# Kernel optimization log

Hardware: AMD Instinct MI355X
Metric: run time of the kernel (lower is better)

## Reference

```python
import jax, jax.numpy as jnp
import numpy as np
from jax import lax

HIDDEN = 256      # hidden_dim
LATENT = 128      # latent_dim
VOCAB = 32000     # vocab_size
MAX_LEN = 64      # max_len (stack capacity guard, as in original)
MAX_STEPS = 128   # fixed step budget for the decode stack machine
N_NODES = 511     # complete binary tree, depth 9


def _linear_params(key, fan_in, fan_out):
    k1, k2 = jax.random.split(key)
    s = 1.0 / np.sqrt(fan_in)
    W = jax.random.uniform(k1, (fan_out, fan_in), minval=-s, maxval=s, dtype=jnp.float32)
    b = jax.random.uniform(k2, (fan_out,), minval=-s, maxval=s, dtype=jnp.float32)
    return W, b


def setup_inputs() -> dict:
    key = jax.random.key(0)
    ks = jax.random.split(key, 10)
    embed = jax.random.normal(ks[0], (VOCAB, HIDDEN), dtype=jnp.float32)
    Wpar, bpar = _linear_params(ks[1], 3 * HIDDEN, HIDDEN)
    Wmu, bmu = _linear_params(ks[2], HIDDEN, LATENT)
    Wlv, blv = _linear_params(ks[3], HIDDEN, LATENT)
    W1, b1 = _linear_params(ks[4], LATENT, HIDDEN)
    W2, b2 = _linear_params(ks[5], HIDDEN, HIDDEN + 1)
    Wl, bl = _linear_params(ks[6], HIDDEN, VOCAB)
    Wp, bp = _linear_params(ks[7], HIDDEN, 2 * LATENT + VOCAB)
    values = jax.random.randint(ks[8], (N_NODES,), 0, VOCAB)
    idx = np.arange(N_NODES)
    left = np.where(2 * idx + 1 < N_NODES, 2 * idx + 1, -1).astype(np.int32)
    right = np.where(2 * idx + 2 < N_NODES, 2 * idx + 2, -1).astype(np.int32)
    eps = jax.random.normal(ks[9], (LATENT,), dtype=jnp.float32)
    return dict(embed=embed, Wpar=Wpar, bpar=bpar, Wmu=Wmu, bmu=bmu,
                Wlv=Wlv, blv=blv, W1=W1, b1=b1, W2=W2, b2=b2,
                Wl=Wl, bl=bl, Wp=Wp, bp=bp, eps=eps,
                values=jnp.asarray(values), left=jnp.asarray(left), right=jnp.asarray(right))


def reference(embed, Wpar, bpar, Wmu, bmu, Wlv, blv, W1, b1, W2, b2,
              Wl, bl, Wp, bp, eps, values, left, right):
    # ---------- encode: bottom-up over tree stored as index arrays ----------
    emb = embed[values]  # [N, H], one gather for all node embeddings

    def enc_step(h, i):
        v = emb[i]
        li = jnp.maximum(left[i], 0)
        ri = jnp.maximum(right[i], 0)
        cat = jnp.concatenate([v, h[li], h[ri]])          # [3H]
        hp = cat @ Wpar.T + bpar                           # parent combine
        hi = jnp.where(left[i] < 0, v, hp)                 # leaf -> embedding
        return h.at[i].set(hi), None

    h0 = jnp.zeros((values.shape[0], HIDDEN), dtype=embed.dtype)
    # children have larger index than parents -> process in descending order
    h, _ = lax.scan(enc_step, h0, jnp.arange(values.shape[0] - 1, -1, -1))
    root = h[0]
    mu = root @ Wmu.T + bmu
    logvar = root @ Wlv.T + blv
    z = mu + eps * jnp.exp(0.5 * logvar)                   # reparameterize

    # ---------- decode: stack machine with fixed step budget ----------
    V, L = VOCAB, LATENT
    stack0 = jnp.zeros((MAX_LEN, L), dtype=z.dtype).at[0].set(z)
    out0 = jnp.zeros((MAX_STEPS, V), dtype=z.dtype)

    def dec_step(state, _):
        stack, sp, out, op = state
        active = sp > 0
        idx = jnp.maximum(sp - 1, 0)
        node = stack[idx]                                  # pop
        hmid = jax.nn.leaky_relu(node @ W1.T + b1, 0.2)
        co = hmid @ W2.T + b2                              # [H+1]; co[0] = gate
        is_parent = (co[0] > 0) & (sp - 1 <= MAX_LEN - 2) & active

        def parent_fn(_):
            dec = co[1:] @ Wp.T + bp                       # [V + 2L]
            value = dec[:V]
            ll = dec[V:V + L]
            rl = dec[V + L:]
            # original appends llatent then rlatent -> rlatent on top
            st = stack.at[idx].set(ll).at[idx + 1].set(rl)
            return value, st, sp + 1

        def leaf_fn(_):
            return co[1:] @ Wl.T + bl, stack, sp - 1

        value, st, nsp = lax.cond(is_parent, parent_fn, leaf_fn, None)
        m = active.astype(z.dtype)
        out = out.at[op].add(m * value)                    # rows written once
        stack = jnp.where(active, st, stack)
        sp = jnp.where(active, nsp, sp)
        op = op + active.astype(op.dtype)
        return (stack, sp, out, op), None

    init = (stack0, jnp.int32(1), out0, jnp.int32(0))
    (_, _, out, _), _ = lax.scan(dec_step, init, None, length=MAX_STEPS)
    return out, mu, logvar
```

## Files before the change

### kernel.cpp

```cpp
#include <hip/hip_runtime.h>

#define HID 256
#define LAT 128
#define VOC 32000
#define NSTEP 128

__global__ __launch_bounds__(512)
void prep_kernel(const float* __restrict__ Wp, const float* __restrict__ W2,
                 const float* __restrict__ b2, const float* __restrict__ bp,
                 const float* __restrict__ Wpar,
                 const float* __restrict__ Wmu, const float* __restrict__ Wlv,
                 float* __restrict__ Wcomb, float* __restrict__ bcomb,
                 float* __restrict__ Wq_par, float* __restrict__ Wq_mu,
                 float* __restrict__ Wq_lv, float* __restrict__ Wq_w2) {
    const int b = blockIdx.x;
    const int t = threadIdx.x;
    if (b < 256) {
        const int o = b;
        const int k = t & 255, jh = t >> 8;
        __shared__ float wpt_s[256];
        __shared__ float part_s[2][256];
        __shared__ float red_s[4];
        if (t < 256) wpt_s[t] = Wp[(size_t)(VOC + o) * HID + t];
        __syncthreads();
        float acc = 0.f;
#pragma unroll 8
        for (int j = 0; j < 128; j++)
            acc += wpt_s[jh * 128 + j] * W2[(size_t)(1 + jh * 128 + j) * HID + k];
        part_s[jh][k] = acc;
        if (t < 256) {
            float p = wpt_s[k] * b2[1 + k];
            p += __shfl_xor(p, 1);  p += __shfl_xor(p, 2);  p += __shfl_xor(p, 4);
            p += __shfl_xor(p, 8);  p += __shfl_xor(p, 16); p += __shfl_xor(p, 32);
            if ((k & 63) == 0) red_s[k >> 6] = p;
        }
        __syncthreads();
        if (t < 256) Wcomb[(size_t)o * HID + k] = part_s[0][k] + part_s[1][k];
        if (t == 0) bcomb[o] = bp[VOC + o] + red_s[0] + red_s[1] + red_s[2] + red_s[3];
    } else if (b < 352) {
        const int k4 = (b - 256) * 2 + (t >> 8);
        const int r = t & 255;
        ((float4*)Wq_par)[k4 * 256 + r] = *(const float4*)(Wpar + (size_t)r * 768 + 4 * k4);
    } else if (b < 384) {
        const int k4 = (b - 352) * 2 + (t >> 8);
        const int r = t & 127, sel = (t >> 7) & 1;
        const float* src = (sel ? Wlv : Wmu) + (size_t)r * HID + 4 * k4;
        ((float4*)(sel ? Wq_lv : Wq_mu))[k4 * 128 + r] = *(const float4*)src;
    } else {
        const int k4 = (b - 384) * 2 + (t >> 8);
        const int r = t & 255;
        ((float4*)Wq_w2)[k4 * 256 + r] = *(const float4*)(W2 + (size_t)(1 + r) * HID + 4 * k4);
    }
}

__global__ __launch_bounds__(1024)
void enc2(const float* __restrict__ embed, const int* __restrict__ values,
          const float* __restrict__ Wq, const float* __restrict__ bpar,
          float* __restrict__ h, int base) {
    const int i = base + blockIdx.x;
    const int t = threadIdx.x;
    const int o = t & 255;
    const int g = t >> 8;
    const int cid = g & 1, kh = g >> 1;
    __shared__ __align__(16) float cat[2][768];
    __shared__ float part[4][256];
    __shared__ __align__(16) float pcat[768];

    const int c0n = 2 * i + 1;
    for (int q = t; q < 1536; q += 1024) {
        const int cc = (q >= 768);
        const int e = q - cc * 768;
        const int node = c0n + cc;
        const int seg = e >> 8, idx = e & 255;
        float v;
        if (seg == 0) v = embed[(size_t)values[node] * HID + idx];
        else {
            const int ch = 2 * node + seg;
            v = (ch >= 255) ? embed[(size_t)values[ch] * HID + idx]
                            : h[(size_t)ch * HID + idx];
        }
        cat[cc][e] = v;
    }
    __syncthreads();
    {
        const float4* wq = (const float4*)Wq + o;
        const float4* c4 = (const float4*)cat[cid] + kh * 96;
        float acc = 0.f;
#pragma unroll 16
        for (int k4 = 0; k4 < 96; k4++) {
            const float4 w = wq[(size_t)(kh * 96 + k4) * 256];
            const float4 cc = c4[k4];
            acc += w.x * cc.x + w.y * cc.y + w.z * cc.z + w.w * cc.w;
        }
        part[g][o] = acc;
    }
    __syncthreads();
    if (t < 512) {
        const int c = t >> 8;
        pcat[256 + (c << 8) + o] = part[c][o] + part[c + 2][o] + bpar[o];
    } else if (t < 768) {
        const int idx = t & 255;
        pcat[idx] = embed[(size_t)values[i] * HID + idx];
    }
    __syncthreads();
    {
        const float4* wq = (const float4*)Wq + o;
        const float4* c4 = (const float4*)pcat + g * 48;
        float acc = 0.f;
#pragma unroll 16
        for (int k4 = 0; k4 < 48; k4++) {
            const float4 w = wq[(size_t)(g * 48 + k4) * 256];
            const float4 cc = c4[k4];
            acc += w.x * cc.x + w.y * cc.y + w.z * cc.z + w.w * cc.w;
        }
        part[g][o] = acc;
    }
    __syncthreads();
    if (t < 256)
        h[(size_t)i * HID + t] = part[0][t] + part[1][t] + part[2][t] + part[3][t] + bpar[t];
}

__global__ __launch_bounds__(1024)
void enc_final(const float* __restrict__ embed, const int* __restrict__ values,
               const float* __restrict__ Wq, const float* __restrict__ bpar,
               const float* __restrict__ h,
               const float* __restrict__ Wq_mu, const float* __restrict__ bmu,
               const float* __restrict__ Wq_lv, const float* __restrict__ blv,
               const float* __restrict__ eps,
               float* __restrict__ out, float* __restrict__ z) {
    const int t = threadIdx.x;
    const int o = t & 255;
    const int g = t >> 8;
    const int cid = g & 1, kh = g >> 1;
    __shared__ __align__(16) float cat[2][768];
    __shared__ float part[4][256];
    __shared__ __align__(16) float pcat[768];
    __shared__ __align__(16) float r0[256];
    __shared__ float mu_s[128], lv_s[128];

    for (int q = t; q < 1536; q += 1024) {
        const int cc = (q >= 768);
        const int e = q - cc * 768;
        const int node = 1 + cc;
        const int seg = e >> 8, idx = e & 255;
        cat[cc][e] = (seg == 0) ? embed[(size_t)values[node] * HID + idx]
                                : h[(size_t)(2 * node + seg) * HID + idx];
    }
    __syncthreads();
    {
        const float4* wq = (const float4*)Wq + o;
        const float4* c4 = (const float4*)cat[cid] + kh * 96;
        float acc = 0.f;
#pragma unroll 16
        for (int k4 = 0; k4 < 96; k4++) {
            const float4 w = wq[(size_t)(kh * 96 + k4) * 256];
            const float4 cc = c4[k4];
            acc += w.x * cc.x + w.y * cc.y + w.z * cc.z + w.w * cc.w;
        }
        part[g][o] = acc;
    }
    __syncthreads();
    if (t < 512) {
        const int c = t >> 8;
        pcat[256 + (c << 8) + o] = part[c][o] + part[c + 2][o] + bpar[o];
    } else if (t < 768) {
        const int idx = t & 255;
        pcat[idx] = embed[(size_t)values[0] * HID + idx];
    }
    __syncthreads();
    {
        const float4* wq = (const float4*)Wq + o;
        const float4* c4 = (const float4*)pcat + g * 48;
        float acc = 0.f;
#pragma unroll 16
        for (int k4 = 0; k4 < 48; k4++) {
            const float4 w = wq[(size_t)(g * 48 + k4) * 256];
            const float4 cc = c4[k4];
            acc += w.x * cc.x + w.y * cc.y + w.z * cc.z + w.w * cc.w;
        }
        part[g][o] = acc;
    }
    __syncthreads();
    if (t < 256)
        r0[t] = part[0][t] + part[1][t] + part[2][t] + part[3][t] + bpar[t];
    __syncthreads();
    {
        const int r = o & 127;
        const float4* wqh = (const float4*)(o < 128 ? Wq_mu : Wq_lv) + r;
        const float4* r4 = (const float4*)r0 + g * 16;
        float acc = 0.f;
#pragma unroll 16
        for (int k4 = 0; k4 < 16; k4++) {
            const float4 w = wqh[(size_t)(g * 16 + k4) * 128];
            const float4 cc = r4[k4];
            acc += w.x * cc.x + w.y * cc.y + w.z * cc.z + w.w * cc.w;
        }
        part[g][o] = acc;
    }
    __syncthreads();
    if (t < 256) {
        const int r = t & 127;
        float v = part[0][t] + part[1][t] + part[2][t] + part[3][t];
        if (t < 128) { v += bmu[r]; out[(size_t)NSTEP * VOC + r] = v;       mu_s[r] = v; }
        else         { v += blv[r]; out[(size_t)NSTEP * VOC + 128 + r] = v; lv_s[r] = v; }
    }
    __syncthreads();
    if (t < 128) z[t] = mu_s[t] + eps[t] * expf(0.5f * lv_s[t]);
}

__global__ __launch_bounds__(512, 2)
void recur_kernel(const float* W1, const float* b1,
                  const float* W2, const float* b2,
                  const float* Wcomb, const float* bcomb,
                  const float* z,
                  float* Hrec, int* rowflag) {
    const int t = threadIdx.x;
    const int o = t >> 1;
    const int hk = t & 1;
    __shared__ __align__(16) float stack_s[64 * 128];
    __shared__ __align__(16) float hmid_s[256];

    float4 w1r[16];
#pragma unroll
    for (int j = 0; j < 16; j++)
        w1r[j] = *(const float4*)(W1 + (size_t)o * 128 + hk * 64 + 4 * j);
    float4 wcr[32];
#pragma unroll
    for (int j = 0; j < 32; j++)
        wcr[j] = *(const float4*)(Wcomb + (size_t)o * 256 + hk * 128 + 4 * j);

    const float b1o = b1[o];
    const float bco = bcomb[o];
    const float b20 = b2[0];
    const int l64 = t & 63;
    const float4 w2q = *(const float4*)(W2 + 4 * l64);

    if (t < 128) stack_s[t] = z[t];
    int sp = 1, op = 0;
    unsigned long long pm0 = 0ULL, pm1 = 0ULL;
    __syncthreads();

    for (int step = 0; step < NSTEP; step++) {
        if (sp <= 0) break;
        const int idx = sp - 1;

        const float* np = stack_s + idx * 128 + hk * 64;
        float a = 0.f;
#pragma unroll
        for (int j = 0; j < 16; j++) {
            const float4 v = *(const float4*)(np + 4 * j);
            a += w1r[j].x * v.x + w1r[j].y * v.y + w1r[j].z * v.z + w1r[j].w * v.w;
        }
        a += __shfl_xor(a, 1);
        if (hk == 0) {
            float pre = a + b1o;
            pre = pre > 0.f ? pre : 0.2f * pre;
            hmid_s[o] = pre;
            Hrec[(size_t)op * HID + o] = pre;
        }
        __syncthreads();

        const float4 hq = *(const float4*)(hmid_s + 4 * l64);
        float c = w2q.x * hq.x + w2q.y * hq.y + w2q.z * hq.z + w2q.w * hq.w;
        c += __shfl_xor(c, 1);  c += __shfl_xor(c, 2);  c += __shfl_xor(c, 4);
        c += __shfl_xor(c, 8);  c += __shfl_xor(c, 16); c += __shfl_xor(c, 32);
        const bool par = ((c + b20) > 0.f) && (sp <= 63);

        if (par) {
            const float* hp = hmid_s + hk * 128;
            float s = 0.f;
#pragma unroll
            for (int j = 0; j < 32; j++) {
                const float4 v = *(const float4*)(hp + 4 * j);
                s += wcr[j].x * v.x + wcr[j].y * v.y + wcr[j].z * v.z + wcr[j].w * v.w;
            }
            s += __shfl_xor(s, 1);
            if (hk == 0)
                stack_s[(idx + (o >> 7)) * 128 + (o & 127)] = s + bco;
            if (op < 64) pm0 |= (1ULL << op); else pm1 |= (1ULL << (op - 64));
            sp += 1;
        } else {
            sp -= 1;
        }
        op++;
        __syncthreads();
    }

    if (t < 128) {
        int f = -1;
        if (t < op) f = (t < 64) ? (int)((pm0 >> t) & 1) : (int)((pm1 >> (t - 64)) & 1);
        rowflag[t] = f;
    }
}

__global__ __launch_bounds__(256)
void co1_kernel(const float* __restrict__ Hrec, const float* __restrict__ Wq_w2,
                const float* __restrict__ b2, float* __restrict__ Co1) {
    const int r = blockIdx.x;
    const int c = threadIdx.x;
    __shared__ __align__(16) float hs[256];
    hs[c] = Hrec[(size_t)r * HID + c];
    __syncthreads();
    float acc = b2[1 + c];
    const float4* wq = (const float4*)Wq_w2 + c;
    const float4* h4 = (const float4*)hs;
#pragma unroll 8
    for (int k4 = 0; k4 < 64; k4++) {
        const float4 a = wq[k4 * 256];
        const float4 hv = h4[k4];
        acc += a.x * hv.x + a.y * hv.y + a.z * hv.z + a.w * hv.w;
    }
    Co1[(size_t)r * HID + c] = acc;
}

__global__ __launch_bounds__(256, 1)
void value_kernel(const float* __restrict__ Co1, const int* __restrict__ rowflag,
                  const float* __restrict__ Wl, const float* __restrict__ bl,
                  const float* __restrict__ Wp, const float* __restrict__ bp,
                  float* __restrict__ out) {
    const int m = blockIdx.y;
    const int t = threadIdx.x;
    const int v = blockIdx.x * 256 + t;
    __shared__ int list_s[128];
    __shared__ int zlist_s[128];
    __shared__ int nn_s, nz_s;
    if (t == 0) {
        int n = 0, znum = 0;
        for (int r = 0; r < 128; r++) {
            const int f = rowflag[r];
            if (f == m) list_s[n++] = r;
            else if (m == 0 && f == -1) zlist_s[znum++] = r;
        }
        nn_s = n; nz_s = znum;
    }
    __syncthreads();
    const int n = nn_s;
    const float* Wx = m ? Wp : Wl;
    const float* bx = m ? bp : bl;
    const float bv = bx[v];
    const float4* w4 = (const float4*)(Wx + (size_t)v * HID);

    for (int rc = 0; rc < n; rc += 32) {
        const int nr = min(32, n - rc);
        float acc[32];
#pragma unroll
        for (int rr = 0; rr < 32; rr++) acc[rr] = 0.f;
        for (int kc = 0; kc < 4; kc++) {
            float4 w[16];
#pragma unroll
            for (int i = 0; i < 16; i++) w[i] = w4[kc * 16 + i];
            for (int rr = 0; rr < nr; rr++) {
                const int row = __builtin_amdgcn_readfirstlane(list_s[rc + rr]);
                const float* cp = Co1 + (size_t)row * HID + kc * 64;
                float s = 0.f;
#pragma unroll
                for (int i = 0; i < 16; i++) {
                    const float4 c4 = *(const float4*)(cp + 4 * i);
                    s += w[i].x * c4.x + w[i].y * c4.y + w[i].z * c4.z + w[i].w * c4.w;
                }
                acc[rr] += s;
            }
        }
        for (int rr = 0; rr < nr; rr++) {
            const int row = __builtin_amdgcn_readfirstlane(list_s[rc + rr]);
            out[(size_t)row * VOC + v] = acc[rr] + bv;
        }
    }
    if (m == 0) {
        const int nz = nz_s;
        for (int i = 0; i < nz; i++) {
            const int row = __builtin_amdgcn_readfirstlane(zlist_s[i]);
            out[(size_t)row * VOC + v] = 0.f;
        }
    }
}

extern "C" void kernel_launch(void* const* d_in, const int* in_sizes, int n_in,
                              void* d_out, int out_size, void* d_ws, size_t ws_size,
                              hipStream_t stream) {
    const float* embed = (const float*)d_in[0];
    const float* Wpar  = (const float*)d_in[1];
    const float* bpar  = (const float*)d_in[2];
    const float* Wmu   = (const float*)d_in[3];
    const float* bmu   = (const float*)d_in[4];
    const float* Wlv   = (const float*)d_in[5];
    const float* blv   = (const float*)d_in[6];
    const float* W1    = (const float*)d_in[7];
    const float* b1    = (const float*)d_in[8];
    const float* W2    = (const float*)d_in[9];
    const float* b2    = (const float*)d_in[10];
    const float* Wl    = (const float*)d_in[11];
    const float* bl    = (const float*)d_in[12];
    const float* Wp    = (const float*)d_in[13];
    const float* bp    = (const float*)d_in[14];
    const float* eps   = (const float*)d_in[15];
    const int*  values = (const int*)d_in[16];

    float* ws = (float*)d_ws;
    float* h       = ws;
    float* z       = ws + 65280;
    float* Wcomb   = ws + 65408;
    float* bcomb   = ws + 130944;
    float* Hrec    = ws + 131200;
    float* Co1     = ws + 163968;
    int*   rowflag = (int*)(ws + 196736);
    float* Wq_par  = ws + 196864;
    float* Wq_mu   = ws + 393472;
    float* Wq_lv   = ws + 426240;
    float* Wq_w2   = ws + 459008;
    float* out = (float*)d_out;

    prep_kernel<<<416, 512, 0, stream>>>(Wp, W2, b2, bp, Wpar, Wmu, Wlv,
                                         Wcomb, bcomb, Wq_par, Wq_mu, Wq_lv, Wq_w2);

    enc2<<<64, 1024, 0, stream>>>(embed, values, Wq_par, bpar, h, 63);
    enc2<<<16, 1024, 0, stream>>>(embed, values, Wq_par, bpar, h, 15);
    enc2<<< 4, 1024, 0, stream>>>(embed, values, Wq_par, bpar, h,  3);
    enc_final<<<1, 1024, 0, stream>>>(embed, values, Wq_par, bpar, h,
                                      Wq_mu, bmu, Wq_lv, blv, eps, out, z);

    recur_kernel<<<1, 512, 0, stream>>>(W1, b1, W2, b2, Wcomb, bcomb, z, Hrec, rowflag);

    co1_kernel<<<128, 256, 0, stream>>>(Hrec, Wq_w2, b2, Co1);
    value_kernel<<<dim3(125, 2), 256, 0, stream>>>(Co1, rowflag, Wl, bl, Wp, bp, out);
}
```

Measured before the change: 281.2 us.

## Split dot-product accumulators, precompute row lists, and double value-kernel grid

Every dot-product loop (encoder, recurrence, co1, value) now uses several independent fmaf accumulators to shorten the serial add chains. Building the row lists by a single thread moves out of each value_kernel block into an extra block of co1_kernel, which writes them to workspace. value_kernel now covers 128 vocab columns per block and splits rows across two thread halves, doubling the grid to fill more compute units. The trade-offs are a different float summation order and more redundant weight loads per column, since both thread halves load the same weights.

```diff
diff --git a/kernel.cpp b/kernel.cpp
--- a/kernel.cpp
+++ b/kernel.cpp
@@ -85,14 +85,24 @@
     {
         const float4* wq = (const float4*)Wq + o;
         const float4* c4 = (const float4*)cat[cid] + kh * 96;
-        float acc = 0.f;
-#pragma unroll 16
-        for (int k4 = 0; k4 < 96; k4++) {
-            const float4 w = wq[(size_t)(kh * 96 + k4) * 256];
-            const float4 cc = c4[k4];
-            acc += w.x * cc.x + w.y * cc.y + w.z * cc.z + w.w * cc.w;
-        }
-        part[g][o] = acc;
+        float s0 = 0.f, s1 = 0.f, s2 = 0.f, s3 = 0.f;
+#pragma unroll 8
+        for (int k4 = 0; k4 < 96; k4 += 4) {
+            const float4 wa = wq[(size_t)(kh * 96 + k4) * 256];
+            const float4 wb = wq[(size_t)(kh * 96 + k4 + 1) * 256];
+            const float4 wc = wq[(size_t)(kh * 96 + k4 + 2) * 256];
+            const float4 wd = wq[(size_t)(kh * 96 + k4 + 3) * 256];
+            const float4 ca = c4[k4], cb = c4[k4 + 1], cx = c4[k4 + 2], cd = c4[k4 + 3];
+            s0 = fmaf(wa.x, ca.x, s0); s0 = fmaf(wa.y, ca.y, s0);
+            s0 = fmaf(wa.z, ca.z, s0); s0 = fmaf(wa.w, ca.w, s0);
+            s1 = fmaf(wb.x, cb.x, s1); s1 = fmaf(wb.y, cb.y, s1);
+            s1 = fmaf(wb.z, cb.z, s1); s1 = fmaf(wb.w, cb.w, s1);
+            s2 = fmaf(wc.x, cx.x, s2); s2 = fmaf(wc.y, cx.y, s2);
+            s2 = fmaf(wc.z, cx.z, s2); s2 = fmaf(wc.w, cx.w, s2);
+            s3 = fmaf(wd.x, cd.x, s3); s3 = fmaf(wd.y, cd.y, s3);
+            s3 = fmaf(wd.z, cd.z, s3); s3 = fmaf(wd.w, cd.w, s3);
+        }
+        part[g][o] = (s0 + s1) + (s2 + s3);
     }
     __syncthreads();
     if (t < 512) {
@@ -106,14 +116,24 @@
     {
         const float4* wq = (const float4*)Wq + o;
         const float4* c4 = (const float4*)pcat + g * 48;
-        float acc = 0.f;
-#pragma unroll 16
-        for (int k4 = 0; k4 < 48; k4++) {
-            const float4 w = wq[(size_t)(g * 48 + k4) * 256];
-            const float4 cc = c4[k4];
-            acc += w.x * cc.x + w.y * cc.y + w.z * cc.z + w.w * cc.w;
-        }
-        part[g][o] = acc;
+        float s0 = 0.f, s1 = 0.f, s2 = 0.f, s3 = 0.f;
+#pragma unroll
+        for (int k4 = 0; k4 < 48; k4 += 4) {
+            const float4 wa = wq[(size_t)(g * 48 + k4) * 256];
+            const float4 wb = wq[(size_t)(g * 48 + k4 + 1) * 256];
+            const float4 wc = wq[(size_t)(g * 48 + k4 + 2) * 256];
+            const float4 wd = wq[(size_t)(g * 48 + k4 + 3) * 256];
+            const float4 ca = c4[k4], cb = c4[k4 + 1], cx = c4[k4 + 2], cd = c4[k4 + 3];
+            s0 = fmaf(wa.x, ca.x, s0); s0 = fmaf(wa.y, ca.y, s0);
+            s0 = fmaf(wa.z, ca.z, s0); s0 = fmaf(wa.w, ca.w, s0);
+            s1 = fmaf(wb.x, cb.x, s1); s1 = fmaf(wb.y, cb.y, s1);
+            s1 = fmaf(wb.z, cb.z, s1); s1 = fmaf(wb.w, cb.w, s1);
+            s2 = fmaf(wc.x, cx.x, s2); s2 = fmaf(wc.y, cx.y, s2);
+            s2 = fmaf(wc.z, cx.z, s2); s2 = fmaf(wc.w, cx.w, s2);
+            s3 = fmaf(wd.x, cd.x, s3); s3 = fmaf(wd.y, cd.y, s3);
+            s3 = fmaf(wd.z, cd.z, s3); s3 = fmaf(wd.w, cd.w, s3);
+        }
+        part[g][o] = (s0 + s1) + (s2 + s3);
     }
     __syncthreads();
     if (t < 256)
@@ -150,14 +170,24 @@
     {
         const float4* wq = (const float4*)Wq + o;
         const float4* c4 = (const float4*)cat[cid] + kh * 96;
-        float acc = 0.f;
-#pragma unroll 16
-        for (int k4 = 0; k4 < 96; k4++) {
-            const float4 w = wq[(size_t)(kh * 96 + k4) * 256];
-            const float4 cc = c4[k4];
-            acc += w.x * cc.x + w.y * cc.y + w.z * cc.z + w.w * cc.w;
-        }
-        part[g][o] = acc;
+        float s0 = 0.f, s1 = 0.f, s2 = 0.f, s3 = 0.f;
+#pragma unroll 8
+        for (int k4 = 0; k4 < 96; k4 += 4) {
+            const float4 wa = wq[(size_t)(kh * 96 + k4) * 256];
+            const float4 wb = wq[(size_t)(kh * 96 + k4 + 1) * 256];
+            const float4 wc = wq[(size_t)(kh * 96 + k4 + 2) * 256];
+            const float4 wd = wq[(size_t)(kh * 96 + k4 + 3) * 256];
+            const float4 ca = c4[k4], cb = c4[k4 + 1], cx = c4[k4 + 2], cd = c4[k4 + 3];
+            s0 = fmaf(wa.x, ca.x, s0); s0 = fmaf(wa.y, ca.y, s0);
+            s0 = fmaf(wa.z, ca.z, s0); s0 = fmaf(wa.w, ca.w, s0);
+            s1 = fmaf(wb.x, cb.x, s1); s1 = fmaf(wb.y, cb.y, s1);
+            s1 = fmaf(wb.z, cb.z, s1); s1 = fmaf(wb.w, cb.w, s1);
+            s2 = fmaf(wc.x, cx.x, s2); s2 = fmaf(wc.y, cx.y, s2);
+            s2 = fmaf(wc.z, cx.z, s2); s2 = fmaf(wc.w, cx.w, s2);
+            s3 = fmaf(wd.x, cd.x, s3); s3 = fmaf(wd.y, cd.y, s3);
+            s3 = fmaf(wd.z, cd.z, s3); s3 = fmaf(wd.w, cd.w, s3);
+        }
+        part[g][o] = (s0 + s1) + (s2 + s3);
     }
     __syncthreads();
     if (t < 512) {
@@ -171,14 +201,24 @@
     {
         const float4* wq = (const float4*)Wq + o;
         const float4* c4 = (const float4*)pcat + g * 48;
-        float acc = 0.f;
-#pragma unroll 16
-        for (int k4 = 0; k4 < 48; k4++) {
-            const float4 w = wq[(size_t)(g * 48 + k4) * 256];
-            const float4 cc = c4[k4];
-            acc += w.x * cc.x + w.y * cc.y + w.z * cc.z + w.w * cc.w;
-        }
-        part[g][o] = acc;
+        float s0 = 0.f, s1 = 0.f, s2 = 0.f, s3 = 0.f;
+#pragma unroll
+        for (int k4 = 0; k4 < 48; k4 += 4) {
+            const float4 wa = wq[(size_t)(g * 48 + k4) * 256];
+            const float4 wb = wq[(size_t)(g * 48 + k4 + 1) * 256];
+            const float4 wc = wq[(size_t)(g * 48 + k4 + 2) * 256];
+            const float4 wd = wq[(size_t)(g * 48 + k4 + 3) * 256];
+            const float4 ca = c4[k4], cb = c4[k4 + 1], cx = c4[k4 + 2], cd = c4[k4 + 3];
+            s0 = fmaf(wa.x, ca.x, s0); s0 = fmaf(wa.y, ca.y, s0);
+            s0 = fmaf(wa.z, ca.z, s0); s0 = fmaf(wa.w, ca.w, s0);
+            s1 = fmaf(wb.x, cb.x, s1); s1 = fmaf(wb.y, cb.y, s1);
+            s1 = fmaf(wb.z, cb.z, s1); s1 = fmaf(wb.w, cb.w, s1);
+            s2 = fmaf(wc.x, cx.x, s2); s2 = fmaf(wc.y, cx.y, s2);
+            s2 = fmaf(wc.z, cx.z, s2); s2 = fmaf(wc.w, cx.w, s2);
+            s3 = fmaf(wd.x, cd.x, s3); s3 = fmaf(wd.y, cd.y, s3);
+            s3 = fmaf(wd.z, cd.z, s3); s3 = fmaf(wd.w, cd.w, s3);
+        }
+        part[g][o] = (s0 + s1) + (s2 + s3);
     }
     __syncthreads();
     if (t < 256)
@@ -188,14 +228,18 @@
         const int r = o & 127;
         const float4* wqh = (const float4*)(o < 128 ? Wq_mu : Wq_lv) + r;
         const float4* r4 = (const float4*)r0 + g * 16;
-        float acc = 0.f;
-#pragma unroll 16
-        for (int k4 = 0; k4 < 16; k4++) {
-            const float4 w = wqh[(size_t)(g * 16 + k4) * 128];
-            const float4 cc = r4[k4];
-            acc += w.x * cc.x + w.y * cc.y + w.z * cc.z + w.w * cc.w;
-        }
-        part[g][o] = acc;
+        float s0 = 0.f, s1 = 0.f;
+#pragma unroll
+        for (int k4 = 0; k4 < 16; k4 += 2) {
+            const float4 wa = wqh[(size_t)(g * 16 + k4) * 128];
+            const float4 wb = wqh[(size_t)(g * 16 + k4 + 1) * 128];
+            const float4 ca = r4[k4], cb = r4[k4 + 1];
+            s0 = fmaf(wa.x, ca.x, s0); s0 = fmaf(wa.y, ca.y, s0);
+            s0 = fmaf(wa.z, ca.z, s0); s0 = fmaf(wa.w, ca.w, s0);
+            s1 = fmaf(wb.x, cb.x, s1); s1 = fmaf(wb.y, cb.y, s1);
+            s1 = fmaf(wb.z, cb.z, s1); s1 = fmaf(wb.w, cb.w, s1);
+        }
+        part[g][o] = s0 + s1;
     }
     __syncthreads();
     if (t < 256) {
@@ -245,12 +289,17 @@
         const int idx = sp - 1;
 
         const float* np = stack_s + idx * 128 + hk * 64;
-        float a = 0.f;
-#pragma unroll
-        for (int j = 0; j < 16; j++) {
-            const float4 v = *(const float4*)(np + 4 * j);
-            a += w1r[j].x * v.x + w1r[j].y * v.y + w1r[j].z * v.z + w1r[j].w * v.w;
-        }
+        float a0 = 0.f, a1 = 0.f;
+#pragma unroll
+        for (int j = 0; j < 16; j += 2) {
+            const float4 v0 = *(const float4*)(np + 4 * j);
+            const float4 v1 = *(const float4*)(np + 4 * j + 4);
+            a0 = fmaf(w1r[j].x, v0.x, a0);     a0 = fmaf(w1r[j].y, v0.y, a0);
+            a0 = fmaf(w1r[j].z, v0.z, a0);     a0 = fmaf(w1r[j].w, v0.w, a0);
+            a1 = fmaf(w1r[j + 1].x, v1.x, a1); a1 = fmaf(w1r[j + 1].y, v1.y, a1);
+            a1 = fmaf(w1r[j + 1].z, v1.z, a1); a1 = fmaf(w1r[j + 1].w, v1.w, a1);
+        }
+        float a = a0 + a1;
         a += __shfl_xor(a, 1);
         if (hk == 0) {
             float pre = a + b1o;
@@ -268,12 +317,23 @@
 
         if (par) {
             const float* hp = hmid_s + hk * 128;
-            float s = 0.f;
-#pragma unroll
-            for (int j = 0; j < 32; j++) {
-                const float4 v = *(const float4*)(hp + 4 * j);
-                s += wcr[j].x * v.x + wcr[j].y * v.y + wcr[j].z * v.z + wcr[j].w * v.w;
+            float s0 = 0.f, s1 = 0.f, s2 = 0.f, s3 = 0.f;
+#pragma unroll
+            for (int j = 0; j < 32; j += 4) {
+                const float4 v0 = *(const float4*)(hp + 4 * j);
+                const float4 v1 = *(const float4*)(hp + 4 * j + 4);
+                const float4 v2 = *(const float4*)(hp + 4 * j + 8);
+                const float4 v3 = *(const float4*)(hp + 4 * j + 12);
+                s0 = fmaf(wcr[j].x, v0.x, s0);     s0 = fmaf(wcr[j].y, v0.y, s0);
+                s0 = fmaf(wcr[j].z, v0.z, s0);     s0 = fmaf(wcr[j].w, v0.w, s0);
+                s1 = fmaf(wcr[j + 1].x, v1.x, s1); s1 = fmaf(wcr[j + 1].y, v1.y, s1);
+                s1 = fmaf(wcr[j + 1].z, v1.z, s1); s1 = fmaf(wcr[j + 1].w, v1.w, s1);
+                s2 = fmaf(wcr[j + 2].x, v2.x, s2); s2 = fmaf(wcr[j + 2].y, v2.y, s2);
+                s2 = fmaf(wcr[j + 2].z, v2.z, s2); s2 = fmaf(wcr[j + 2].w, v2.w, s2);
+                s3 = fmaf(wcr[j + 3].x, v3.x, s3); s3 = fmaf(wcr[j + 3].y, v3.y, s3);
+                s3 = fmaf(wcr[j + 3].z, v3.z, s3); s3 = fmaf(wcr[j + 3].w, v3.w, s3);
             }
+            float s = (s0 + s1) + (s2 + s3);
             s += __shfl_xor(s, 1);
             if (hk == 0)
                 stack_s[(idx + (o >> 7)) * 128 + (o & 127)] = s + bco;
@@ -295,46 +355,58 @@
 
 __global__ __launch_bounds__(256)
 void co1_kernel(const float* __restrict__ Hrec, const float* __restrict__ Wq_w2,
-                const float* __restrict__ b2, float* __restrict__ Co1) {
+                const float* __restrict__ b2, const int* __restrict__ rowflag,
+                float* __restrict__ Co1, int* __restrict__ lists) {
     const int r = blockIdx.x;
     const int c = threadIdx.x;
+    if (r == 128) {
+        if (c == 0) {
+            int nl = 0, np_ = 0, nz = 0;
+            for (int q = 0; q < 128; q++) {
+                const int f = rowflag[q];
+                if (f == 0) lists[nl++] = q;
+                else if (f == 1) lists[128 + np_++] = q;
+                else lists[256 + nz++] = q;
+            }
+            lists[384] = nl; lists[385] = np_; lists[386] = nz;
+        }
+        return;
+    }
     __shared__ __align__(16) float hs[256];
     hs[c] = Hrec[(size_t)r * HID + c];
     __syncthreads();
-    float acc = b2[1 + c];
     const float4* wq = (const float4*)Wq_w2 + c;
     const float4* h4 = (const float4*)hs;
+    float s0 = b2[1 + c], s1 = 0.f, s2 = 0.f, s3 = 0.f;
 #pragma unroll 8
-    for (int k4 = 0; k4 < 64; k4++) {
-        const float4 a = wq[k4 * 256];
-        const float4 hv = h4[k4];
-        acc += a.x * hv.x + a.y * hv.y + a.z * hv.z + a.w * hv.w;
-    }
-    Co1[(size_t)r * HID + c] = acc;
-}
-
-__global__ __launch_bounds__(256, 1)
-void value_kernel(const float* __restrict__ Co1, const int* __restrict__ rowflag,
+    for (int k4 = 0; k4 < 64; k4 += 4) {
+        const float4 a0 = wq[(k4) * 256],     h0 = h4[k4];
+        const float4 a1 = wq[(k4 + 1) * 256], h1 = h4[k4 + 1];
+        const float4 a2 = wq[(k4 + 2) * 256], h2 = h4[k4 + 2];
+        const float4 a3 = wq[(k4 + 3) * 256], h3 = h4[k4 + 3];
+        s0 = fmaf(a0.x, h0.x, s0); s0 = fmaf(a0.y, h0.y, s0);
+        s0 = fmaf(a0.z, h0.z, s0); s0 = fmaf(a0.w, h0.w, s0);
+        s1 = fmaf(a1.x, h1.x, s1); s1 = fmaf(a1.y, h1.y, s1);
+        s1 = fmaf(a1.z, h1.z, s1); s1 = fmaf(a1.w, h1.w, s1);
+        s2 = fmaf(a2.x, h2.x, s2); s2 = fmaf(a2.y, h2.y, s2);
+        s2 = fmaf(a2.z, h2.z, s2); s2 = fmaf(a2.w, h2.w, s2);
+        s3 = fmaf(a3.x, h3.x, s3); s3 = fmaf(a3.y, h3.y, s3);
+        s3 = fmaf(a3.z, h3.z, s3); s3 = fmaf(a3.w, h3.w, s3);
+    }
+    Co1[(size_t)r * HID + c] = (s0 + s1) + (s2 + s3);
+}
+
+__global__ __launch_bounds__(256, 2)
+void value_kernel(const float* __restrict__ Co1, const int* __restrict__ lists,
                   const float* __restrict__ Wl, const float* __restrict__ bl,
                   const float* __restrict__ Wp, const float* __restrict__ bp,
                   float* __restrict__ out) {
     const int m = blockIdx.y;
     const int t = threadIdx.x;
-    const int v = blockIdx.x * 256 + t;
-    __shared__ int list_s[128];
-    __shared__ int zlist_s[128];
-    __shared__ int nn_s, nz_s;
-    if (t == 0) {
-        int n = 0, znum = 0;
-        for (int r = 0; r < 128; r++) {
-            const int f = rowflag[r];
-            if (f == m) list_s[n++] = r;
-            else if (m == 0 && f == -1) zlist_s[znum++] = r;
-        }
-        nn_s = n; nz_s = znum;
-    }
-    __syncthreads();
-    const int n = nn_s;
+    const int v = blockIdx.x * 128 + (t & 127);
+    const int rh = t >> 7;
+    const int n = lists[384 + m];
+    const int* list = lists + m * 128;
     const float* Wx = m ? Wp : Wl;
     const float* bx = m ? bp : bl;
     const float bv = bx[v];
@@ -342,36 +414,53 @@
 
     for (int rc = 0; rc < n; rc += 32) {
         const int nr = min(32, n - rc);
-        float acc[32];
-#pragma unroll
-        for (int rr = 0; rr < 32; rr++) acc[rr] = 0.f;
+        float acc[16];
+#pragma unroll
+        for (int i = 0; i < 16; i++) acc[i] = 0.f;
         for (int kc = 0; kc < 4; kc++) {
             float4 w[16];
 #pragma unroll
             for (int i = 0; i < 16; i++) w[i] = w4[kc * 16 + i];
-            for (int rr = 0; rr < nr; rr++) {
-                const int row = __builtin_amdgcn_readfirstlane(list_s[rc + rr]);
-                const float* cp = Co1 + (size_t)row * HID + kc * 64;
-                float s = 0.f;
-#pragma unroll
-                for (int i = 0; i < 16; i++) {
-                    const float4 c4 = *(const float4*)(cp + 4 * i);
-                    s += w[i].x * c4.x + w[i].y * c4.y + w[i].z * c4.z + w[i].w * c4.w;
+#pragma unroll
+            for (int aa = 0; aa < 16; aa++) {
+                const int rr = 2 * aa + rh;
+                if (rr < nr) {
+                    const int row = __builtin_amdgcn_readfirstlane(list[rc + rr]);
+                    const float* cp = Co1 + (size_t)row * HID + kc * 64;
+                    float s0 = 0.f, s1 = 0.f, s2 = 0.f, s3 = 0.f;
+#pragma unroll
+                    for (int i = 0; i < 16; i += 4) {
+                        const float4 c0 = *(const float4*)(cp + 4 * i);
+                        const float4 c1 = *(const float4*)(cp + 4 * i + 4);
+                        const float4 c2 = *(const float4*)(cp + 4 * i + 8);
+                        const float4 c3 = *(const float4*)(cp + 4 * i + 12);
+                        s0 = fmaf(w[i].x, c0.x, s0);     s0 = fmaf(w[i].y, c0.y, s0);
+                        s0 = fmaf(w[i].z, c0.z, s0);     s0 = fmaf(w[i].w, c0.w, s0);
+                        s1 = fmaf(w[i + 1].x, c1.x, s1); s1 = fmaf(w[i + 1].y, c1.y, s1);
+                        s1 = fmaf(w[i + 1].z, c1.z, s1); s1 = fmaf(w[i + 1].w, c1.w, s1);
+                        s2 = fmaf(w[i + 2].x, c2.x, s2); s2 = fmaf(w[i + 2].y, c2.y, s2);
+                        s2 = fmaf(w[i + 2].z, c2.z, s2); s2 = fmaf(w[i + 2].w, c2.w, s2);
+                        s3 = fmaf(w[i + 3].x, c3.x, s3); s3 = fmaf(w[i + 3].y, c3.y, s3);
+                        s3 = fmaf(w[i + 3].z, c3.z, s3); s3 = fmaf(w[i + 3].w, c3.w, s3);
+                    }
+                    acc[aa] += (s0 + s1) + (s2 + s3);
                 }
-                acc[rr] += s;
             }
         }
-        for (int rr = 0; rr < nr; rr++) {
-            const int row = __builtin_amdgcn_readfirstlane(list_s[rc + rr]);
-            out[(size_t)row * VOC + v] = acc[rr] + bv;
-        }
-    }
-    if (m == 0) {
-        const int nz = nz_s;
-        for (int i = 0; i < nz; i++) {
-            const int row = __builtin_amdgcn_readfirstlane(zlist_s[i]);
-            out[(size_t)row * VOC + v] = 0.f;
-        }
+#pragma unroll
+        for (int aa = 0; aa < 16; aa++) {
+            const int rr = 2 * aa + rh;
+            if (rr < nr) {
+                const int row = __builtin_amdgcn_readfirstlane(list[rc + rr]);
+                out[(size_t)row * VOC + v] = acc[aa] + bv;
+            }
+        }
+    }
+    if (m == 0 && rh == 0) {
+        const int nz = lists[386];
+        const int* zl = lists + 256;
+        for (int i = 0; i < nz; i++)
+            out[(size_t)zl[i] * VOC + v] = 0.f;
     }
 }
 
@@ -408,6 +497,7 @@
     float* Wq_mu   = ws + 393472;
     float* Wq_lv   = ws + 426240;
     float* Wq_w2   = ws + 459008;
+    int*   lists   = (int*)(ws + 524544);
     float* out = (float*)d_out;
 
     prep_kernel<<<416, 512, 0, stream>>>(Wp, W2, b2, bp, Wpar, Wmu, Wlv,
@@ -421,6 +511,6 @@
 
     recur_kernel<<<1, 512, 0, stream>>>(W1, b1, W2, b2, Wcomb, bcomb, z, Hrec, rowflag);
 
-    co1_kernel<<<128, 256, 0, stream>>>(Hrec, Wq_w2, b2, Co1);
-    value_kernel<<<dim3(125, 2), 256, 0, stream>>>(Co1, rowflag, Wl, bl, Wp, bp, out);
-}
+    co1_kernel<<<129, 256, 0, stream>>>(Hrec, Wq_w2, b2, rowflag, Co1, lists);
+    value_kernel<<<dim3(250, 2), 256, 0, stream>>>(Co1, lists, Wl, bl, Wp, bp, out);
+}
```

Result: no change. 277.7 us (-1.2%).
